# Kernel optimization log

Hardware: AMD Instinct MI355X
Metric: run time of the kernel (lower is better)

Reference implementation:

```python
import jax, jax.numpy as jnp
import numpy as np

N, E, K = 1048576, 64, 8        # tokens, experts, top-k
TEMP = 1.0                       # default temperature_scheduler returns 1.0
NEG = -1e16                      # masked-logit fill from the original code
EPS = 1e-8


def setup_inputs() -> dict:
    key = jax.random.key(0)
    k1, k2 = jax.random.split(key)
    inputs = jax.random.normal(k1, (N, E), dtype=jnp.float32)
    # Gumbel noise exactly as sample_gumbel(): -log(-log(U + 1e-8) + 1e-8)
    u = jax.random.uniform(k2, (N, E), dtype=jnp.float32)
    noise = -jnp.log(-jnp.log(u + EPS) + EPS)
    return {"inputs": inputs, "noise": noise}


def reference(inputs, noise):
    # Gumbel-perturbed softmax over experts (training path)
    probs = jax.nn.softmax((inputs + noise) / TEMP, axis=1)          # [N, E]
    # top-k expert selection on perturbed probs (indices only matter)
    _, top_k_idx = jax.lax.top_k(probs, K)                           # [N, K]
    # one-hot-sum mask built via scatter instead of materializing [N, K, E]
    rows = jnp.arange(inputs.shape[0])[:, None]                      # [N, 1]
    mask = jnp.zeros_like(inputs).at[rows, top_k_idx].set(1.0)       # [N, E]
    # keep ORIGINAL (un-noised) logits at selected experts, -1e16 elsewhere
    sparse_inputs = jnp.where(mask > 0.0, inputs, NEG)
    # renormalize over the selected experts
    return jax.nn.softmax(sparse_inputs, axis=1)
```

## Files before the change

### kernel.cpp

```cpp
#include <hip/hip_runtime.h>
#include <cstdint>

#define EXPERTS 64

typedef float float4v __attribute__((ext_vector_type(4)));

__device__ __forceinline__ uint32_t mono32(float x) {
    int32_t b = __float_as_int(x);
    return (uint32_t)(b ^ ((b >> 31) | 0x80000000));
}

__device__ __forceinline__ void gll16(const float* g, float* l) {
    __builtin_amdgcn_global_load_lds((const __attribute__((address_space(1))) void*)g,
                                     (__attribute__((address_space(3))) void*)l, 16, 0, 0);
}

__global__ __launch_bounds__(64, 2)
void gumbel_topk_softmax_kernel(const float* __restrict__ gin,
                                const float* __restrict__ gnz,
                                float* __restrict__ gout) {
    __shared__ __align__(16) float bufA[64 * 64];
    __shared__ __align__(16) float bufB[64 * 64];

    const int t    = threadIdx.x;
    const int row0 = blockIdx.x * 64;
    const int sw   = t & 7;

#pragma unroll
    for (int k = 0; k < 16; ++k) {
        const int p = k * 64 + t;
        const int r = p >> 4;
        const int j = (p & 15) ^ (r & 7);
        const uint32_t gofs = (uint32_t)(row0 + r) * 64u + (uint32_t)j * 4u;
        gll16(gin + gofs, &bufA[k * 256]);
        gll16(gnz + gofs, &bufB[k * 256]);
    }
    __syncthreads();

    float vin[EXPERTS];
    float keys[EXPERTS];
    float heap[8];
#pragma unroll
    for (int q = 0; q < 8; ++q) heap[q] = -INFINITY;

#pragma unroll
    for (int q = 0; q < 16; ++q) {
        const int p = 16 * t + (q ^ sw);
        float4v a = *(const float4v*)&bufA[p * 4];
        float4v b = *(const float4v*)&bufB[p * 4];
#pragma unroll
        for (int i = 0; i < 4; ++i) {
            const int j = q * 4 + i;
            float s = a[i] + b[i];
            vin[j]  = a[i];
            keys[j] = s;
#pragma unroll
            for (int u = 0; u < 8; ++u) {
                float h = heap[u];
                heap[u] = fmaxf(h, s);
                s       = fminf(h, s);
            }
        }
    }

    const float T = heap[7];
    int cnt = 0;
    uint32_t mlo = 0u, mhi = 0u;
#pragma unroll
    for (int j = 0; j < 64; ++j) {
        bool ge = keys[j] >= T;
        cnt += ge ? 1 : 0;
        if (j < 32) mlo |= ge ? (1u << j) : 0u;
        else        mhi |= ge ? (1u << (j - 32)) : 0u;
    }
    if (cnt != 8) {
        unsigned long long h8[8];
#pragma unroll
        for (int q = 0; q < 8; ++q) h8[q] = 0ull;
#pragma unroll
        for (int j = 0; j < 64; ++j) {
            const int p = 16 * t + ((j >> 2) ^ sw);
            float a = vin[j];
            float b = bufB[p * 4 + (j & 3)];
            float s  = a + b;
            float ap = s - b;
            float bp = s - ap;
            float res = (a - ap) + (b - bp);
            unsigned long long key = ((unsigned long long)mono32(s) << 32)
                                   | ((unsigned long long)(mono32(res) >> 6) << 6)
                                   | (unsigned long long)(63 - j);
#pragma unroll
            for (int q = 0; q < 8; ++q) {
                unsigned long long hq = h8[q];
                unsigned long long mx = key > hq ? key : hq;
                key   = key > hq ? hq : key;
                h8[q] = mx;
            }
        }
        mlo = mhi = 0u;
#pragma unroll
        for (int q = 0; q < 8; ++q) {
            int j = 63 - (int)(h8[q] & 63ull);
            if (j < 32) mlo |= 1u << j;
            else        mhi |= 1u << (j - 32);
        }
    }

    float ssum = 0.f;
#pragma unroll
    for (int j = 0; j < 64; ++j) {
        uint32_t bit = (j < 32 ? (mlo >> j) : (mhi >> (j - 32))) & 1u;
        float ev = __expf(vin[j]) * (float)bit;
        ssum += ev;
        vin[j] = ev;
    }
    const float inv = 1.0f / ssum;

#pragma unroll
    for (int q = 0; q < 16; ++q) {
        float4v v;
#pragma unroll
        for (int i = 0; i < 4; ++i) v[i] = vin[q * 4 + i] * inv;
        *(float4v*)&bufA[(16 * t + (q ^ sw)) * 4] = v;
    }
    __syncthreads();
#pragma unroll
    for (int k = 0; k < 16; ++k) {
        const int p = k * 64 + t;
        float4v v = *(const float4v*)&bufA[p * 4];
        const int r  = p >> 4;
        const int jq = (p & 15) ^ (r & 7);
        *(float4v*)(gout + (uint32_t)(row0 + r) * 64u + (uint32_t)jq * 4u) = v;
    }
}

extern "C" void kernel_launch(void* const* d_in, const int* in_sizes, int n_in,
                              void* d_out, int out_size, void* d_ws, size_t ws_size,
                              hipStream_t stream) {
    const float* gin = (const float*)d_in[0];
    const float* gnz = (const float*)d_in[1];
    float* gout = (float*)d_out;
    const int nrows = in_sizes[0] / EXPERTS;
    const int grid  = nrows / 64;
    gumbel_topk_softmax_kernel<<<grid, 64, 0, stream>>>(gin, gnz, gout);
}
```

Baseline: 154.0 us.

## Pipeline column-chunk LDS loads with top-k compute; store output rows directly

Splits the input staging into four 16-column chunks, double-buffered in LDS, so the heap top-k work on one chunk can overlap the global-to-LDS load of the next. The rare tie-break fallback now reads the noise straight from global memory instead of LDS. The output no longer goes back through LDS: each thread writes its own row directly with 16-byte stores. That removes a barrier and the LDS round trip, but each lane now writes a separate 256-byte row, which risks less coalesced stores. Since every barrier likely waits on all outstanding loads, the amount of real overlap may be small.

After: 206.9 us. 34.4% more time.

```diff
diff --git a/kernel.cpp b/kernel.cpp
--- a/kernel.cpp
+++ b/kernel.cpp
@@ -1,7 +1,5 @@
 #include <hip/hip_runtime.h>
 #include <cstdint>
-
-#define EXPERTS 64
 
 typedef float float4v __attribute__((ext_vector_type(4)));
 
@@ -15,53 +13,72 @@
                                      (__attribute__((address_space(3))) void*)l, 16, 0, 0);
 }
 
+
+#define ISSUE_Q(c)                                                             \
+    {                                                                          \
+        _Pragma("unroll")                                                      \
+        for (int k = 0; k < 4; ++k) {                                          \
+            uint32_t gofs = (uint32_t)(row0 + 16 * k + rl) * 64u               \
+                          + (uint32_t)(c) * 16u + (uint32_t)qd * 4u;           \
+            gll16(gin + gofs, &qA[(c) & 1][k * 256]);                          \
+            gll16(gnz + gofs, &qB[(c) & 1][k * 256]);                          \
+        }                                                                      \
+    }
+
+#define CONSUME_Q(c)                                                           \
+    {                                                                          \
+        _Pragma("unroll")                                                      \
+        for (int j = 0; j < 4; ++j) {                                          \
+            const int u = 4 * t + (j ^ sw2);                                   \
+            float4v a = *(const float4v*)&qA[(c) & 1][u * 4];                  \
+            float4v b = *(const float4v*)&qB[(c) & 1][u * 4];                  \
+            _Pragma("unroll")                                                  \
+            for (int i = 0; i < 4; ++i) {                                      \
+                const int e = (c) * 16 + j * 4 + i;                            \
+                float s = a[i] + b[i];                                         \
+                vin[e]  = a[i];                                                \
+                keys[e] = s;                                                   \
+                _Pragma("unroll")                                              \
+                for (int u8 = 0; u8 < 8; ++u8) {                               \
+                    float h = heap[u8];                                        \
+                    heap[u8] = fmaxf(h, s);                                    \
+                    s        = fminf(h, s);                                    \
+                }                                                              \
+            }                                                                  \
+        }                                                                      \
+    }
+
 __global__ __launch_bounds__(64, 2)
 void gumbel_topk_softmax_kernel(const float* __restrict__ gin,
                                 const float* __restrict__ gnz,
                                 float* __restrict__ gout) {
-    __shared__ __align__(16) float bufA[64 * 64];
-    __shared__ __align__(16) float bufB[64 * 64];
+    __shared__ __align__(16) float qA[2][1024];
+    __shared__ __align__(16) float qB[2][1024];
 
     const int t    = threadIdx.x;
     const int row0 = blockIdx.x * 64;
-    const int sw   = t & 7;
+    const int rl   = t >> 2;
+    const int qd   = (t & 3) ^ ((t >> 3) & 3);
+    const int sw2  = (t >> 1) & 3;
 
-#pragma unroll
-    for (int k = 0; k < 16; ++k) {
-        const int p = k * 64 + t;
-        const int r = p >> 4;
-        const int j = (p & 15) ^ (r & 7);
-        const uint32_t gofs = (uint32_t)(row0 + r) * 64u + (uint32_t)j * 4u;
-        gll16(gin + gofs, &bufA[k * 256]);
-        gll16(gnz + gofs, &bufB[k * 256]);
-    }
-    __syncthreads();
-
-    float vin[EXPERTS];
-    float keys[EXPERTS];
+    float vin[64];
+    float keys[64];
     float heap[8];
 #pragma unroll
     for (int q = 0; q < 8; ++q) heap[q] = -INFINITY;
 
-#pragma unroll
-    for (int q = 0; q < 16; ++q) {
-        const int p = 16 * t + (q ^ sw);
-        float4v a = *(const float4v*)&bufA[p * 4];
-        float4v b = *(const float4v*)&bufB[p * 4];
-#pragma unroll
-        for (int i = 0; i < 4; ++i) {
-            const int j = q * 4 + i;
-            float s = a[i] + b[i];
-            vin[j]  = a[i];
-            keys[j] = s;
-#pragma unroll
-            for (int u = 0; u < 8; ++u) {
-                float h = heap[u];
-                heap[u] = fmaxf(h, s);
-                s       = fminf(h, s);
-            }
-        }
-    }
+    ISSUE_Q(0);
+    __syncthreads();
+    ISSUE_Q(1);
+    CONSUME_Q(0);
+    __syncthreads();
+    ISSUE_Q(2);
+    CONSUME_Q(1);
+    __syncthreads();
+    ISSUE_Q(3);
+    CONSUME_Q(2);
+    __syncthreads();
+    CONSUME_Q(3);
 
     const float T = heap[7];
     int cnt = 0;
@@ -77,11 +94,10 @@
         unsigned long long h8[8];
 #pragma unroll
         for (int q = 0; q < 8; ++q) h8[q] = 0ull;
+        const float* brow = gnz + (size_t)(row0 + t) * 64;
 #pragma unroll
         for (int j = 0; j < 64; ++j) {
-            const int p = 16 * t + ((j >> 2) ^ sw);
-            float a = vin[j];
-            float b = bufB[p * 4 + (j & 3)];
+            float a = vin[j], b = brow[j];
             float s  = a + b;
             float ap = s - b;
             float bp = s - ap;
@@ -116,21 +132,13 @@
     }
     const float inv = 1.0f / ssum;
 
+    float4v* orow = (float4v*)(gout + (size_t)(row0 + t) * 64);
 #pragma unroll
     for (int q = 0; q < 16; ++q) {
         float4v v;
 #pragma unroll
         for (int i = 0; i < 4; ++i) v[i] = vin[q * 4 + i] * inv;
-        *(float4v*)&bufA[(16 * t + (q ^ sw)) * 4] = v;
-    }
-    __syncthreads();
-#pragma unroll
-    for (int k = 0; k < 16; ++k) {
-        const int p = k * 64 + t;
-        float4v v = *(const float4v*)&bufA[p * 4];
-        const int r  = p >> 4;
-        const int jq = (p & 15) ^ (r & 7);
-        *(float4v*)(gout + (uint32_t)(row0 + r) * 64u + (uint32_t)jq * 4u) = v;
+        orow[q] = v;
     }
 }
 
@@ -140,7 +148,7 @@
     const float* gin = (const float*)d_in[0];
     const float* gnz = (const float*)d_in[1];
     float* gout = (float*)d_out;
-    const int nrows = in_sizes[0] / EXPERTS;
+    const int nrows = in_sizes[0] / 64;
     const int grid  = nrows / 64;
     gumbel_topk_softmax_kernel<<<grid, 64, 0, stream>>>(gin, gnz, gout);
 }
```

## Load noise directly into registers and store output rows without LDS staging

Applied to the files above, without the earlier changes.

The noise tensor is now read straight from global memory into registers, one full row per thread, instead of being staged through a second LDS buffer. Output rows are likewise written directly from registers rather than transposed back through LDS. This halves LDS usage and drops a barrier, which may allow more resident blocks. The cost is uncoalesced per-thread row accesses (each lane strides 256 bytes) and higher register pressure from holding 64 noise values.

Result: slower. 222.3 us (+44.3%).

```diff
diff --git a/kernel.cpp b/kernel.cpp
--- a/kernel.cpp
+++ b/kernel.cpp
@@ -1,7 +1,5 @@
 #include <hip/hip_runtime.h>
 #include <cstdint>
-
-#define EXPERTS 64
 
 typedef float float4v __attribute__((ext_vector_type(4)));
 
@@ -20,7 +18,6 @@
                                 const float* __restrict__ gnz,
                                 float* __restrict__ gout) {
     __shared__ __align__(16) float bufA[64 * 64];
-    __shared__ __align__(16) float bufB[64 * 64];
 
     const int t    = threadIdx.x;
     const int row0 = blockIdx.x * 64;
@@ -31,34 +28,36 @@
         const int p = k * 64 + t;
         const int r = p >> 4;
         const int j = (p & 15) ^ (r & 7);
-        const uint32_t gofs = (uint32_t)(row0 + r) * 64u + (uint32_t)j * 4u;
-        gll16(gin + gofs, &bufA[k * 256]);
-        gll16(gnz + gofs, &bufB[k * 256]);
+        gll16(gin + (uint32_t)(row0 + r) * 64u + (uint32_t)j * 4u, &bufA[k * 256]);
     }
+    const float4v* nrow = (const float4v*)(gnz + (size_t)(row0 + t) * 64);
+    float4v nz[16];
+#pragma unroll
+    for (int q = 0; q < 16; ++q) nz[q] = nrow[q];
+
     __syncthreads();
 
-    float vin[EXPERTS];
-    float keys[EXPERTS];
+    float vin[64];
+    float keys[64];
     float heap[8];
 #pragma unroll
     for (int q = 0; q < 8; ++q) heap[q] = -INFINITY;
 
 #pragma unroll
     for (int q = 0; q < 16; ++q) {
-        const int p = 16 * t + (q ^ sw);
-        float4v a = *(const float4v*)&bufA[p * 4];
-        float4v b = *(const float4v*)&bufB[p * 4];
+        const int u = 16 * t + (q ^ sw);
+        float4v a = *(const float4v*)&bufA[u * 4];
 #pragma unroll
         for (int i = 0; i < 4; ++i) {
             const int j = q * 4 + i;
-            float s = a[i] + b[i];
+            float s = a[i] + nz[q][i];
             vin[j]  = a[i];
             keys[j] = s;
 #pragma unroll
-            for (int u = 0; u < 8; ++u) {
-                float h = heap[u];
-                heap[u] = fmaxf(h, s);
-                s       = fminf(h, s);
+            for (int u8 = 0; u8 < 8; ++u8) {
+                float h = heap[u8];
+                heap[u8] = fmaxf(h, s);
+                s        = fminf(h, s);
             }
         }
     }
@@ -79,9 +78,7 @@
         for (int q = 0; q < 8; ++q) h8[q] = 0ull;
 #pragma unroll
         for (int j = 0; j < 64; ++j) {
-            const int p = 16 * t + ((j >> 2) ^ sw);
-            float a = vin[j];
-            float b = bufB[p * 4 + (j & 3)];
+            float a = vin[j], b = nz[j >> 2][j & 3];
             float s  = a + b;
             float ap = s - b;
             float bp = s - ap;
@@ -116,21 +113,13 @@
     }
     const float inv = 1.0f / ssum;
 
+    float4v* orow = (float4v*)(gout + (size_t)(row0 + t) * 64);
 #pragma unroll
     for (int q = 0; q < 16; ++q) {
         float4v v;
 #pragma unroll
         for (int i = 0; i < 4; ++i) v[i] = vin[q * 4 + i] * inv;
-        *(float4v*)&bufA[(16 * t + (q ^ sw)) * 4] = v;
-    }
-    __syncthreads();
-#pragma unroll
-    for (int k = 0; k < 16; ++k) {
-        const int p = k * 64 + t;
-        float4v v = *(const float4v*)&bufA[p * 4];
-        const int r  = p >> 4;
-        const int jq = (p & 15) ^ (r & 7);
-        *(float4v*)(gout + (uint32_t)(row0 + r) * 64u + (uint32_t)jq * 4u) = v;
+        orow[q] = v;
     }
 }
 
@@ -140,7 +129,7 @@
     const float* gin = (const float*)d_in[0];
     const float* gnz = (const float*)d_in[1];
     float* gout = (float*)d_out;
-    const int nrows = in_sizes[0] / EXPERTS;
+    const int nrows = in_sizes[0] / 64;
     const int grid  = nrows / 64;
     gumbel_topk_softmax_kernel<<<grid, 64, 0, stream>>>(gin, gnz, gout);
 }
```
